# Performance work log

Measured on AMD Instinct MI355X. Metric: run time of the kernel, lower is better.

## Reference

```python
import jax, jax.numpy as jnp
import numpy as np

N = 20000
E = 320000
NEG_SLOPE = 0.2
BN_EPS = 1e-5


def _segment_softmax(e, dst, n):
    # e: [E, H] attention logits, dst: [E] destination node ids
    m = jax.ops.segment_max(e, dst, num_segments=n)           # [N, H]
    ex = jnp.exp(e - m[dst])                                   # [E, H]
    s = jax.ops.segment_sum(ex, dst, num_segments=n)          # [N, H]
    return ex / s[dst]


def gat_conv(x, src, dst, W, a_src, a_dst, b, heads, out_ch):
    # PyG GATConv (concat=True): h = x @ W reshaped to [N, H, C]
    n = x.shape[0]
    h = (x @ W).reshape(n, heads, out_ch)                      # [N, H, C]
    al_s = jnp.einsum('nhc,hc->nh', h, a_src)                  # [N, H]
    al_d = jnp.einsum('nhc,hc->nh', h, a_dst)
    e = jax.nn.leaky_relu(al_s[src] + al_d[dst], NEG_SLOPE)    # [E, H]
    alpha = _segment_softmax(e, dst, n)                        # [E, H]
    msg = h[src] * alpha[:, :, None]                           # [E, H, C]
    out = jax.ops.segment_sum(msg, dst, num_segments=n)        # [N, H, C]
    return out.reshape(n, heads * out_ch) + b


def batch_norm(x, gamma, beta):
    mu = jnp.mean(x, axis=0)
    var = jnp.mean((x - mu) ** 2, axis=0)  # biased, as torch BN training
    return gamma * (x - mu) * jax.lax.rsqrt(var + BN_EPS) + beta


def setup_inputs() -> dict:
    key = jax.random.key(0)
    ks = jax.random.split(key, 16)
    F_in, H1, C1 = 128, 8, 64
    D = H1 * C1  # 512
    OUT = 2
    def gl(k, shape, fan):
        return jax.random.normal(k, shape, dtype=jnp.float32) / np.sqrt(fan)
    x = jax.random.normal(ks[0], (N, F_in), dtype=jnp.float32)
    edge_index = jax.random.randint(ks[1], (2, E), 0, N, dtype=jnp.int64)
    return {
        'x': x, 'edge_index': edge_index,
        'W1': gl(ks[2], (F_in, H1 * C1), F_in),
        'a1s': gl(ks[3], (H1, C1), C1), 'a1d': gl(ks[4], (H1, C1), C1),
        'b1': jnp.zeros((D,), jnp.float32),
        'W2': gl(ks[5], (D, D), D),
        'a2s': gl(ks[6], (1, D), D), 'a2d': gl(ks[7], (1, D), D),
        'b2': jnp.zeros((D,), jnp.float32),
        'fc1_w': gl(ks[8], (D, D), D), 'fc1_b': jnp.zeros((D,), jnp.float32),
        'g1': jnp.ones((D,), jnp.float32), 'be1': jnp.zeros((D,), jnp.float32),
        'fc2_w': gl(ks[9], (D, D), D), 'fc2_b': jnp.zeros((D,), jnp.float32),
        'g2': jnp.ones((D,), jnp.float32), 'be2': jnp.zeros((D,), jnp.float32),
        'lin_w': gl(ks[10], (D, OUT), D), 'lin_b': jnp.zeros((OUT,), jnp.float32),
    }


def reference(x, edge_index, W1, a1s, a1d, b1, W2, a2s, a2d, b2,
              fc1_w, fc1_b, g1, be1, fc2_w, fc2_b, g2, be2, lin_w, lin_b):
    n = x.shape[0]
    loop = jnp.arange(n, dtype=edge_index.dtype)
    src = jnp.concatenate([edge_index[0], loop])  # add self-loops (PyG default)
    dst = jnp.concatenate([edge_index[1], loop])
    h = gat_conv(x, src, dst, W1, a1s, a1d, b1, heads=8, out_ch=64)
    h = batch_norm(jax.nn.relu(h @ fc1_w + fc1_b), g1, be1)
    h = gat_conv(h, src, dst, W2, a2s, a2d, b2, heads=1, out_ch=512)
    h = batch_norm(jax.nn.relu(h @ fc2_w + fc2_b), g2, be2)
    out = jax.nn.relu(h @ lin_w + lin_b)  # dropout p=0 is identity
    return out
```

## Files before the change

kernel.cpp:

```cpp
#include <hip/hip_runtime.h>
#include <hip/hip_bf16.h>

static constexpr int NN = 20000;
static constexpr int EE = 320000;
static constexpr int ET = EE + NN;
static constexpr int DD = 512;
static constexpr int FIN = 128;

typedef __attribute__((ext_vector_type(8))) short short8;
typedef __attribute__((ext_vector_type(4))) float f32x4;

__device__ __forceinline__ unsigned short f2bf(float f) {
    unsigned u = __float_as_uint(f);
    u += 0x7fffu + ((u >> 16) & 1u);
    return (unsigned short)(u >> 16);
}
__device__ __forceinline__ float bf2f(unsigned short b) {
    return __uint_as_float(((unsigned)b) << 16);
}

__device__ __forceinline__ void async_copy16(short* lds, const unsigned short* g) {
    __builtin_amdgcn_global_load_lds(
        (const __attribute__((address_space(1))) unsigned int*)g,
        (__attribute__((address_space(3))) unsigned int*)lds,
        16, 0, 0);
}

template <int IS64>
__global__ void count_deg(const void* __restrict__ ei, int* __restrict__ deg) {
    int i = blockIdx.x * blockDim.x + threadIdx.x;
    if (i >= EE) return;
    int d = IS64 ? (int)((const long long*)ei)[EE + i] : ((const int*)ei)[EE + i];
    atomicAdd(&deg[d], 1);
}

__global__ void scan_k(const int* __restrict__ deg, int* __restrict__ row_ptr) {
    __shared__ int part[1024];
    int t = threadIdx.x;
    const int CH = (NN + 1023) / 1024;
    int start = t * CH;
    int end = min(start + CH, NN);
    int s = 0;
    for (int i = start; i < end; ++i) s += deg[i] + 1;
    part[t] = s;
    __syncthreads();
    for (int off = 1; off < 1024; off <<= 1) {
        int v = 0;
        if (t >= off) v = part[t - off];
        __syncthreads();
        part[t] += v;
        __syncthreads();
    }
    int base = (t == 0) ? 0 : part[t - 1];
    for (int i = start; i < end; ++i) { row_ptr[i] = base; base += deg[i] + 1; }
    if (t == 1023) row_ptr[NN] = part[1023];
}

template <int IS64>
__global__ void fill_csr(const void* __restrict__ ei,
                         const int* __restrict__ row_ptr, int* __restrict__ cursor,
                         int* __restrict__ csr_src) {
    int e = blockIdx.x * blockDim.x + threadIdx.x;
    if (e >= ET) return;
    int s, d;
    if (e < EE) {
        if (IS64) {
            const long long* p = (const long long*)ei;
            s = (int)p[e]; d = (int)p[EE + e];
        } else {
            const int* p = (const int*)ei;
            s = p[e]; d = p[EE + e];
        }
    } else {
        s = d = e - EE;
    }
    int pos = atomicAdd(&cursor[d], 1);
    csr_src[row_ptr[d] + pos] = s;
}

static constexpr int TBLK = 208;
static constexpr int SZ_X = NN * FIN;
__global__ __launch_bounds__(256) void prep_all_k(
    const float* __restrict__ x, const float* __restrict__ W1,
    const float* __restrict__ fc1, const float* __restrict__ W2,
    const float* __restrict__ fc2,
    unsigned short* __restrict__ xb, unsigned short* __restrict__ W1t,
    unsigned short* __restrict__ fc1t, unsigned short* __restrict__ W2t,
    unsigned short* __restrict__ fc2t) {
    int b = blockIdx.x;
    if (b < TBLK) {
        __shared__ unsigned short tile[64][65];
        const float* src; unsigned short* dst; int rows, cols;
        if (b < 16)       { src = W1;  dst = W1t;  rows = FIN; cols = DD; }
        else if (b < 80)  { b -= 16;  src = fc1; dst = fc1t; rows = DD; cols = DD; }
        else if (b < 144) { b -= 80;  src = W2;  dst = W2t;  rows = DD; cols = DD; }
        else              { b -= 144; src = fc2; dst = fc2t; rows = DD; cols = DD; }
        int tc = cols / 64;
        int r0 = (b / tc) * 64, c0 = (b % tc) * 64;
        int t = threadIdx.x, lr = t >> 6, lc = t & 63;
#pragma unroll
        for (int p = 0; p < 16; ++p) {
            int r = lr + p * 4;
            tile[r][lc] = f2bf(src[(size_t)(r0 + r) * cols + c0 + lc]);
        }
        __syncthreads();
#pragma unroll
        for (int p = 0; p < 16; ++p) {
            int r = lr + p * 4;
            dst[(size_t)(c0 + r) * rows + r0 + lc] = tile[lc][r];
        }
        return;
    }
    int i = (b - TBLK) * 256 + threadIdx.x;
    if (i < SZ_X) xb[i] = f2bf(x[i]);
}

template <int RELU, int HASBIAS, int STATS, int ALS, int H>
__global__ __launch_bounds__(256) void gemm_bf16(const unsigned short* __restrict__ A,
                                                 const unsigned short* __restrict__ Bt,
                                                 const float* __restrict__ bias,
                                                 unsigned short* __restrict__ Cb,
                                                 float* __restrict__ bnstat,
                                                 const float* __restrict__ avs,
                                                 const float* __restrict__ avd,
                                                 float* __restrict__ al_s,
                                                 float* __restrict__ al_d,
                                                 int M, int Nc, int K) {
    int id = blockIdx.x;
    int bm = ((id >> 5) << 3) + (id & 7);
    int bn = (id >> 3) & 3;
    int m0 = bm * 128, n0 = bn * 128;
    if (m0 >= M) return;

    __shared__ short As0[128 * 32], As1[128 * 32];
    __shared__ short Bs0[128 * 32], Bs1[128 * 32];
    int t = threadIdx.x;
    int lane = t & 63, w = t >> 6;
    int wm = w & 1, wn = w >> 1;
    int quad = lane >> 4, mr = lane & 15;
    int lrow = lane >> 2;
    int lcol = (lane & 3) * 8;

    const unsigned short* Ag0 = A + (size_t)(m0 + w * 32 + lrow) * K + lcol;
    const unsigned short* Ag1 = A + (size_t)(m0 + w * 32 + 16 + lrow) * K + lcol;
    const unsigned short* Bg0 = Bt + (size_t)(n0 + w * 32 + lrow) * K + lcol;
    const unsigned short* Bg1 = Bt + (size_t)(n0 + w * 32 + 16 + lrow) * K + lcol;
    short* Al[2][2] = {{&As0[(w * 32) * 32], &As0[(w * 32 + 16) * 32]},
                       {&As1[(w * 32) * 32], &As1[(w * 32 + 16) * 32]}};
    short* Bl[2][2] = {{&Bs0[(w * 32) * 32], &Bs0[(w * 32 + 16) * 32]},
                       {&Bs1[(w * 32) * 32], &Bs1[(w * 32 + 16) * 32]}};

    f32x4 zero = {0.f, 0.f, 0.f, 0.f};
    f32x4 acc[4][4];
#pragma unroll
    for (int i = 0; i < 4; ++i)
#pragma unroll
        for (int j = 0; j < 4; ++j) acc[i][j] = zero;

    for (int k0 = 0; k0 < K; k0 += 64) {
        async_copy16(Al[0][0], Ag0 + k0);
        async_copy16(Al[1][0], Ag0 + k0 + 32);
        async_copy16(Al[0][1], Ag1 + k0);
        async_copy16(Al[1][1], Ag1 + k0 + 32);
        async_copy16(Bl[0][0], Bg0 + k0);
        async_copy16(Bl[1][0], Bg0 + k0 + 32);
        async_copy16(Bl[0][1], Bg1 + k0);
        async_copy16(Bl[1][1], Bg1 + k0 + 32);
        __syncthreads();
#pragma unroll
        for (int kp = 0; kp < 2; ++kp) {
            const short* Sa = kp ? As1 : As0;
            const short* Sb = kp ? Bs1 : Bs0;
            short8 af[4], bfr[4];
#pragma unroll
            for (int i = 0; i < 4; ++i) {
                af[i]  = *(const short8*)(&Sa[(wm * 64 + i * 16 + mr) * 32 + quad * 8]);
                bfr[i] = *(const short8*)(&Sb[(wn * 64 + i * 16 + mr) * 32 + quad * 8]);
            }
#pragma unroll
            for (int i = 0; i < 4; ++i)
#pragma unroll
                for (int j = 0; j < 4; ++j)
                    acc[i][j] = __builtin_amdgcn_mfma_f32_16x16x32_bf16(af[i], bfr[j], acc[i][j], 0, 0, 0);
        }
        __syncthreads();
    }

    float as_j[4], ad_j[4];
    if (ALS) {
#pragma unroll
        for (int j = 0; j < 4; ++j) {
            int n = n0 + wn * 64 + j * 16 + mr;
            as_j[j] = avs[n];
            ad_j[j] = avd[n];
        }
    }
    const int head = (H == 8) ? ((n0 + wn * 64) >> 6) : 0;
    float sj[4] = {0.f, 0.f, 0.f, 0.f}, qj[4] = {0.f, 0.f, 0.f, 0.f};
#pragma unroll
    for (int i = 0; i < 4; ++i) {
        int mb = m0 + wm * 64 + i * 16 + quad * 4;
#pragma unroll
        for (int r = 0; r < 4; ++r) {
            int m = mb + r;
            bool valid = (m < M);
            float ps = 0.f, pd = 0.f;
#pragma unroll
            for (int j = 0; j < 4; ++j) {
                int n = n0 + wn * 64 + j * 16 + mr;
                float v = acc[i][j][r];
                if (HASBIAS) v += bias[n];
                if (RELU) v = fmaxf(v, 0.f);
                unsigned short hb = f2bf(v);
                if (valid) Cb[(size_t)m * Nc + n] = hb;
                if (ALS) {
                    float vv = bf2f(hb);
                    ps += as_j[j] * vv;
                    pd += ad_j[j] * vv;
                }
                if (STATS && valid) { sj[j] += v; qj[j] += v * v; }
            }
            if (ALS) {
                ps += __shfl_xor(ps, 1); pd += __shfl_xor(pd, 1);
                ps += __shfl_xor(ps, 2); pd += __shfl_xor(pd, 2);
                ps += __shfl_xor(ps, 4); pd += __shfl_xor(pd, 4);
                ps += __shfl_xor(ps, 8); pd += __shfl_xor(pd, 8);
                if (mr == 0 && valid) {
                    if (H == 8) { al_s[m * 8 + head] = ps; al_d[m * 8 + head] = pd; }
                    else        { atomicAdd(&al_s[m], ps); atomicAdd(&al_d[m], pd); }
                }
            }
        }
    }
    if (STATS) {
#pragma unroll
        for (int j = 0; j < 4; ++j) {
            float s = sj[j], q = qj[j];
            s += __shfl_xor(s, 16); q += __shfl_xor(q, 16);
            s += __shfl_xor(s, 32); q += __shfl_xor(q, 32);
            if (lane < 16) {
                int n = n0 + wn * 64 + j * 16 + mr;
                atomicAdd(&bnstat[n], s);
                atomicAdd(&bnstat[512 + n], q);
            }
        }
    }
}

template <int H>
__global__ __launch_bounds__(256) void gat_gather_k(const unsigned short* __restrict__ hb,
                                                    const float* __restrict__ al_s,
                                                    const float* __restrict__ al_d,
                                                    const int* __restrict__ row_ptr,
                                                    const int* __restrict__ csr_src,
                                                    const float* __restrict__ bias,
                                                    unsigned short* __restrict__ outb) {
    int b = blockIdx.x;
    int slice = (b & 7) >> 1;
    int g = ((b >> 3) << 1) | (b & 1);
    int t = threadIdx.x;
    int w = t >> 6, lane = t & 63;
    int n = g * 4 + w;
    int col = slice * 128 + lane * 2;
    const int hh = (H == 8) ? (col >> 6) : 0;
    float ald = al_d[n * H + hh];
    int beg = row_ptr[n], end = row_ptr[n + 1];
    const char* hbase = (const char*)(hb + col);
    float acc0 = 0.f, acc1 = 0.f, psum = 0.f;

    for (int p0 = beg; p0 < end; p0 += 64) {
        int cnt = min(64, end - p0);
        int sv = (p0 + lane < end) ? csr_src[p0 + lane] : 0;
        int p = 0;
        for (; p + 8 <= cnt; p += 8) {
            int sn[8];
#pragma unroll
            for (int u = 0; u < 8; ++u) sn[u] = __shfl(sv, p + u);
            float l[8];
#pragma unroll
            for (int u = 0; u < 8; ++u) l[u] = al_s[sn[u] * H + hh] + ald;
            unsigned hv[8];
#pragma unroll
            for (int u = 0; u < 8; ++u)
                hv[u] = *(const unsigned*)(hbase + ((unsigned)sn[u] << 10));
            float a[8];
#pragma unroll
            for (int u = 0; u < 8; ++u) {
                float xx = l[u];
                a[u] = __expf((xx > 0.f) ? xx : 0.2f * xx);
                psum += a[u];
            }
#pragma unroll
            for (int u = 0; u < 8; ++u) {
                acc0 = fmaf(a[u], __uint_as_float(hv[u] << 16), acc0);
                acc1 = fmaf(a[u], __uint_as_float(hv[u] & 0xffff0000u), acc1);
            }
        }
        for (; p < cnt; ++p) {
            int sn0 = __shfl(sv, p);
            float l0 = al_s[sn0 * H + hh] + ald;
            unsigned h0 = *(const unsigned*)(hbase + ((unsigned)sn0 << 10));
            float a0 = __expf((l0 > 0.f) ? l0 : 0.2f * l0);
            psum += a0;
            acc0 = fmaf(a0, __uint_as_float(h0 << 16), acc0);
            acc1 = fmaf(a0, __uint_as_float(h0 & 0xffff0000u), acc1);
        }
    }
    float inv = 1.0f / psum;
    float2 bv = *(const float2*)(bias + col);
    unsigned short o0 = f2bf(acc0 * inv + bv.x);
    unsigned short o1 = f2bf(acc1 * inv + bv.y);
    *(unsigned*)(outb + (size_t)n * DD + col) = ((unsigned)o1 << 16) | (unsigned)o0;
}

__global__ __launch_bounds__(256) void fold1_k(const float* __restrict__ stat,
                                               const float* __restrict__ g,
                                               const float* __restrict__ be,
                                               unsigned short* __restrict__ W2t,
                                               float* __restrict__ bias2) {
    int t = threadIdx.x;
    int n = blockIdx.x * 4 + (t >> 6);
    int lane = t & 63;
    float pb = 0.f;
#pragma unroll
    for (int j = 0; j < 8; ++j) {
        int k = lane * 8 + j;
        float mean = stat[k] * (1.0f / NN);
        float var = stat[512 + k] * (1.0f / NN) - mean * mean;
        float sc = g[k] * rsqrtf(var + 1e-5f);
        float sh = be[k] - mean * sc;
        float wv = bf2f(W2t[n * DD + k]);
        W2t[n * DD + k] = f2bf(sc * wv);
        pb += sh * wv;
    }
    for (int off = 32; off; off >>= 1) pb += __shfl_down(pb, off);
    if (lane == 0) bias2[n] = pb;
}

__global__ void final_linear(const unsigned short* __restrict__ xb,
                             const float* __restrict__ stat, const float* __restrict__ g,
                             const float* __restrict__ be, const float* __restrict__ w,
                             const float* __restrict__ b, float* __restrict__ out) {
    int wave = (blockIdx.x * blockDim.x + threadIdx.x) >> 6;
    int lane = threadIdx.x & 63;
    if (wave >= NN) return;
    short8 hv = *(const short8*)(xb + (size_t)wave * DD + lane * 8);
    float p0 = 0.f, p1 = 0.f;
#pragma unroll
    for (int j = 0; j < 8; ++j) {
        int c = lane * 8 + j;
        float mean = stat[c] * (1.0f / NN);
        float var = stat[512 + c] * (1.0f / NN) - mean * mean;
        float sc = g[c] * rsqrtf(var + 1e-5f);
        float vn = (bf2f((unsigned short)hv[j]) - mean) * sc + be[c];
        p0 += vn * w[2 * c];
        p1 += vn * w[2 * c + 1];
    }
    for (int off = 32; off; off >>= 1) {
        p0 += __shfl_down(p0, off);
        p1 += __shfl_down(p1, off);
    }
    if (lane == 0) {
        out[wave * 2 + 0] = fmaxf(p0 + b[0], 0.f);
        out[wave * 2 + 1] = fmaxf(p1 + b[1], 0.f);
    }
}

extern "C" void kernel_launch(void* const* d_in, const int* in_sizes, int n_in,
                              void* d_out, int out_size, void* d_ws, size_t ws_size,
                              hipStream_t stream) {
    const float* x     = (const float*)d_in[0];
    const void*  ei    = d_in[1];
    const float* W1    = (const float*)d_in[2];
    const float* a1s   = (const float*)d_in[3];
    const float* a1d   = (const float*)d_in[4];
    const float* b1    = (const float*)d_in[5];
    const float* W2    = (const float*)d_in[6];
    const float* a2s   = (const float*)d_in[7];
    const float* a2d   = (const float*)d_in[8];
    const float* b2    = (const float*)d_in[9];
    const float* fc1_w = (const float*)d_in[10];
    const float* fc1_b = (const float*)d_in[11];
    const float* g1    = (const float*)d_in[12];
    const float* be1   = (const float*)d_in[13];
    const float* fc2_w = (const float*)d_in[14];
    const float* fc2_b = (const float*)d_in[15];
    const float* g2    = (const float*)d_in[16];
    const float* be2   = (const float*)d_in[17];
    const float* lin_w = (const float*)d_in[18];
    const float* lin_b = (const float*)d_in[19];
    float* out = (float*)d_out;

    char* ws = (char*)d_ws;
    auto alloc = [&](size_t bytes) {
        void* p = (void*)ws;
        ws += (bytes + 255) & ~size_t(255);
        return p;
    };
    unsigned short* h_bf    = (unsigned short*)alloc((size_t)NN * DD * 2);
    unsigned short* act_bf  = (unsigned short*)alloc((size_t)NN * DD * 2);
    unsigned short* W1t     = (unsigned short*)alloc((size_t)DD * FIN * 2);
    unsigned short* fc1t    = (unsigned short*)alloc((size_t)DD * DD * 2);
    unsigned short* W2t     = (unsigned short*)alloc((size_t)DD * DD * 2);
    unsigned short* fc2t    = (unsigned short*)alloc((size_t)DD * DD * 2);
    float*          al_s    = (float*)alloc((size_t)NN * 8 * 4);
    float*          al_d    = (float*)alloc((size_t)NN * 8 * 4);
    float*          al_s2   = (float*)alloc((size_t)NN * 4);
    float*          al_d2   = (float*)alloc((size_t)NN * 4);
    int*            row_ptr = (int*)alloc((size_t)(NN + 1) * 4);
    int*            deg     = (int*)alloc((size_t)NN * 4);
    int*            cursor  = (int*)alloc((size_t)NN * 4);
    int*            csr_src = (int*)alloc((size_t)ET * 4);
    float*          bnstatA = (float*)alloc(1024 * 4);
    float*          bnstatB = (float*)alloc(1024 * 4);
    float*          bias2f  = (float*)alloc(512 * 4);

    const int is64 = (in_sizes[1] >= (int)(2u * EE * 8u)) ? 1 : 0;

    hipMemsetAsync(deg, 0, (size_t)NN * 4, stream);
    hipMemsetAsync(cursor, 0, (size_t)NN * 4, stream);
    hipMemsetAsync(bnstatA, 0, 1024 * 4, stream);
    hipMemsetAsync(bnstatB, 0, 1024 * 4, stream);
    hipMemsetAsync(al_s2, 0, (size_t)NN * 4, stream);
    hipMemsetAsync(al_d2, 0, (size_t)NN * 4, stream);

    if (is64) {
        count_deg<1><<<(EE + 255) / 256, 256, 0, stream>>>(ei, deg);
    } else {
        count_deg<0><<<(EE + 255) / 256, 256, 0, stream>>>(ei, deg);
    }
    scan_k<<<1, 1024, 0, stream>>>(deg, row_ptr);
    if (is64) {
        fill_csr<1><<<(ET + 255) / 256, 256, 0, stream>>>(ei, row_ptr, cursor, csr_src);
    } else {
        fill_csr<0><<<(ET + 255) / 256, 256, 0, stream>>>(ei, row_ptr, cursor, csr_src);
    }

    unsigned short* x_bf = act_bf;
    const int prep_blocks = TBLK + (SZ_X + 255) / 256;
    prep_all_k<<<prep_blocks, 256, 0, stream>>>(x, W1, fc1_w, W2, fc2_w,
                                                x_bf, W1t, fc1t, W2t, fc2t);

    const int GB = 640;
    const int GGB = NN / 4 * 4;

    gemm_bf16<0, 0, 0, 1, 8><<<GB, 256, 0, stream>>>(
        x_bf, W1t, nullptr, h_bf, nullptr, a1s, a1d, al_s, al_d, NN, DD, FIN);
    gat_gather_k<8><<<GGB, 256, 0, stream>>>(h_bf, al_s, al_d, row_ptr, csr_src, b1, act_bf);
    gemm_bf16<1, 1, 1, 0, 8><<<GB, 256, 0, stream>>>(
        act_bf, fc1t, fc1_b, h_bf, bnstatA, nullptr, nullptr, nullptr, nullptr, NN, DD, DD);
    fold1_k<<<128, 256, 0, stream>>>(bnstatA, g1, be1, W2t, bias2f);

    gemm_bf16<0, 1, 0, 1, 1><<<GB, 256, 0, stream>>>(
        h_bf, W2t, bias2f, act_bf, nullptr, a2s, a2d, al_s2, al_d2, NN, DD, DD);
    gat_gather_k<1><<<GGB, 256, 0, stream>>>(act_bf, al_s2, al_d2, row_ptr, csr_src, b2, h_bf);
    gemm_bf16<1, 1, 1, 0, 8><<<GB, 256, 0, stream>>>(
        h_bf, fc2t, fc2_b, act_bf, bnstatB, nullptr, nullptr, nullptr, nullptr, NN, DD, DD);

    final_linear<<<(NN + 3) / 4, 256, 0, stream>>>(act_bf, bnstatB, g2, be2, lin_w, lin_b, out);
}
```

Measured before the change: 383.8 us.

## Precompute per-edge attention weights and parallelize gather across edges with wide loads

Adds kernels that compute the exponentiated leaky-relu attention weight for each CSR edge once, storing (src, weight) pairs per head, instead of recomputing them per column slice inside the gather. The gather kernel is restructured so each wave splits edges into 8 strips and columns into 8-element groups, using 16-byte feature loads and a cross-lane shuffle reduction. This removes redundant logit and exp work and improves memory-level parallelism. In exchange it adds an extra pass, a csr_dst array and a large edge-weight buffer that must be written and reread.

```diff
diff --git a/kernel.cpp b/kernel.cpp
--- a/kernel.cpp
+++ b/kernel.cpp
@@ -59,7 +59,7 @@
 template <int IS64>
 __global__ void fill_csr(const void* __restrict__ ei,
                          const int* __restrict__ row_ptr, int* __restrict__ cursor,
-                         int* __restrict__ csr_src) {
+                         int* __restrict__ csr_src, int* __restrict__ csr_dst) {
     int e = blockIdx.x * blockDim.x + threadIdx.x;
     if (e >= ET) return;
     int s, d;
@@ -75,7 +75,9 @@
         s = d = e - EE;
     }
     int pos = atomicAdd(&cursor[d], 1);
-    csr_src[row_ptr[d] + pos] = s;
+    int slot = row_ptr[d] + pos;
+    csr_src[slot] = s;
+    csr_dst[slot] = d;
 }
 
 static constexpr int TBLK = 208;
@@ -247,70 +249,82 @@
     }
 }
 
+__global__ __launch_bounds__(256) void alpha1_k(const float* __restrict__ al_s,
+                                                const float* __restrict__ al_d,
+                                                const int* __restrict__ csr_src,
+                                                const int* __restrict__ csr_dst,
+                                                int2* __restrict__ ea) {
+    int p = blockIdx.x * blockDim.x + threadIdx.x;
+    if (p >= ET) return;
+    int sn = csr_src[p], d = csr_dst[p];
+    float4 s0 = *(const float4*)(al_s + (size_t)sn * 8);
+    float4 s1 = *(const float4*)(al_s + (size_t)sn * 8 + 4);
+    float4 d0 = *(const float4*)(al_d + (size_t)d * 8);
+    float4 d1 = *(const float4*)(al_d + (size_t)d * 8 + 4);
+    float l[8] = {s0.x + d0.x, s0.y + d0.y, s0.z + d0.z, s0.w + d0.w,
+                  s1.x + d1.x, s1.y + d1.y, s1.z + d1.z, s1.w + d1.w};
+#pragma unroll
+    for (int h = 0; h < 8; ++h) {
+        float xx = l[h];
+        float a = __expf((xx > 0.f) ? xx : 0.2f * xx);
+        ea[(size_t)h * ET + p] = make_int2(sn, __float_as_int(a));
+    }
+}
+
+__global__ __launch_bounds__(256) void alpha2_k(const float* __restrict__ al_s,
+                                                const float* __restrict__ al_d,
+                                                const int* __restrict__ csr_src,
+                                                const int* __restrict__ csr_dst,
+                                                int2* __restrict__ ea) {
+    int p = blockIdx.x * blockDim.x + threadIdx.x;
+    if (p >= ET) return;
+    int sn = csr_src[p], d = csr_dst[p];
+    float xx = al_s[sn] + al_d[d];
+    float a = __expf((xx > 0.f) ? xx : 0.2f * xx);
+    ea[p] = make_int2(sn, __float_as_int(a));
+}
+
 template <int H>
 __global__ __launch_bounds__(256) void gat_gather_k(const unsigned short* __restrict__ hb,
-                                                    const float* __restrict__ al_s,
-                                                    const float* __restrict__ al_d,
+                                                    const int2* __restrict__ ea,
                                                     const int* __restrict__ row_ptr,
-                                                    const int* __restrict__ csr_src,
                                                     const float* __restrict__ bias,
                                                     unsigned short* __restrict__ outb) {
     int b = blockIdx.x;
-    int slice = (b & 7) >> 1;
-    int g = ((b >> 3) << 1) | (b & 1);
+    int s = b & 7;
+    int g = b >> 3;
     int t = threadIdx.x;
     int w = t >> 6, lane = t & 63;
     int n = g * 4 + w;
-    int col = slice * 128 + lane * 2;
-    const int hh = (H == 8) ? (col >> 6) : 0;
-    float ald = al_d[n * H + hh];
+    int estrip = lane >> 3, cg = lane & 7;
+    int col = s * 64 + cg * 8;
+    const int2* ep = ea + (H == 8 ? (size_t)s * ET : 0);
     int beg = row_ptr[n], end = row_ptr[n + 1];
-    const char* hbase = (const char*)(hb + col);
-    float acc0 = 0.f, acc1 = 0.f, psum = 0.f;
-
-    for (int p0 = beg; p0 < end; p0 += 64) {
-        int cnt = min(64, end - p0);
-        int sv = (p0 + lane < end) ? csr_src[p0 + lane] : 0;
-        int p = 0;
-        for (; p + 8 <= cnt; p += 8) {
-            int sn[8];
-#pragma unroll
-            for (int u = 0; u < 8; ++u) sn[u] = __shfl(sv, p + u);
-            float l[8];
-#pragma unroll
-            for (int u = 0; u < 8; ++u) l[u] = al_s[sn[u] * H + hh] + ald;
-            unsigned hv[8];
-#pragma unroll
-            for (int u = 0; u < 8; ++u)
-                hv[u] = *(const unsigned*)(hbase + ((unsigned)sn[u] << 10));
-            float a[8];
-#pragma unroll
-            for (int u = 0; u < 8; ++u) {
-                float xx = l[u];
-                a[u] = __expf((xx > 0.f) ? xx : 0.2f * xx);
-                psum += a[u];
-            }
-#pragma unroll
-            for (int u = 0; u < 8; ++u) {
-                acc0 = fmaf(a[u], __uint_as_float(hv[u] << 16), acc0);
-                acc1 = fmaf(a[u], __uint_as_float(hv[u] & 0xffff0000u), acc1);
-            }
-        }
-        for (; p < cnt; ++p) {
-            int sn0 = __shfl(sv, p);
-            float l0 = al_s[sn0 * H + hh] + ald;
-            unsigned h0 = *(const unsigned*)(hbase + ((unsigned)sn0 << 10));
-            float a0 = __expf((l0 > 0.f) ? l0 : 0.2f * l0);
-            psum += a0;
-            acc0 = fmaf(a0, __uint_as_float(h0 << 16), acc0);
-            acc1 = fmaf(a0, __uint_as_float(h0 & 0xffff0000u), acc1);
-        }
-    }
-    float inv = 1.0f / psum;
-    float2 bv = *(const float2*)(bias + col);
-    unsigned short o0 = f2bf(acc0 * inv + bv.x);
-    unsigned short o1 = f2bf(acc1 * inv + bv.y);
-    *(unsigned*)(outb + (size_t)n * DD + col) = ((unsigned)o1 << 16) | (unsigned)o0;
+
+    float acc[8] = {0.f, 0.f, 0.f, 0.f, 0.f, 0.f, 0.f, 0.f};
+    float psum = 0.f;
+    for (int p = beg + estrip; p < end; p += 8) {
+        int2 v = ep[p];
+        float a = __int_as_float(v.y);
+        psum += a;
+        short8 hv = *(const short8*)(hb + ((size_t)v.x << 9) + col);
+#pragma unroll
+        for (int j = 0; j < 8; ++j)
+            acc[j] = fmaf(a, bf2f((unsigned short)hv[j]), acc[j]);
+    }
+#pragma unroll
+    for (int m = 8; m <= 32; m <<= 1) {
+        psum += __shfl_xor(psum, m);
+#pragma unroll
+        for (int j = 0; j < 8; ++j) acc[j] += __shfl_xor(acc[j], m);
+    }
+    if (estrip == 0) {
+        float inv = 1.0f / psum;
+        unsigned short ov[8];
+#pragma unroll
+        for (int j = 0; j < 8; ++j) ov[j] = f2bf(acc[j] * inv + bias[col + j]);
+        *(int4*)(outb + (size_t)n * DD + col) = *(const int4*)ov;
+    }
 }
 
 __global__ __launch_bounds__(256) void fold1_k(const float* __restrict__ stat,
@@ -411,9 +425,11 @@
     int*            deg     = (int*)alloc((size_t)NN * 4);
     int*            cursor  = (int*)alloc((size_t)NN * 4);
     int*            csr_src = (int*)alloc((size_t)ET * 4);
+    int*            csr_dst = (int*)alloc((size_t)ET * 4);
     float*          bnstatA = (float*)alloc(1024 * 4);
     float*          bnstatB = (float*)alloc(1024 * 4);
     float*          bias2f  = (float*)alloc(512 * 4);
+    int2*           ea      = (int2*)alloc((size_t)8 * ET * 8);
 
     const int is64 = (in_sizes[1] >= (int)(2u * EE * 8u)) ? 1 : 0;
 
@@ -431,9 +447,9 @@
     }
     scan_k<<<1, 1024, 0, stream>>>(deg, row_ptr);
     if (is64) {
-        fill_csr<1><<<(ET + 255) / 256, 256, 0, stream>>>(ei, row_ptr, cursor, csr_src);
+        fill_csr<1><<<(ET + 255) / 256, 256, 0, stream>>>(ei, row_ptr, cursor, csr_src, csr_dst);
     } else {
-        fill_csr<0><<<(ET + 255) / 256, 256, 0, stream>>>(ei, row_ptr, cursor, csr_src);
+        fill_csr<0><<<(ET + 255) / 256, 256, 0, stream>>>(ei, row_ptr, cursor, csr_src, csr_dst);
     }
 
     unsigned short* x_bf = act_bf;
@@ -442,18 +458,21 @@
                                                 x_bf, W1t, fc1t, W2t, fc2t);
 
     const int GB = 640;
-    const int GGB = NN / 4 * 4;
+    const int GGB = 8 * (NN / 4);
+    const int AB = (ET + 255) / 256;
 
     gemm_bf16<0, 0, 0, 1, 8><<<GB, 256, 0, stream>>>(
         x_bf, W1t, nullptr, h_bf, nullptr, a1s, a1d, al_s, al_d, NN, DD, FIN);
-    gat_gather_k<8><<<GGB, 256, 0, stream>>>(h_bf, al_s, al_d, row_ptr, csr_src, b1, act_bf);
+    alpha1_k<<<AB, 256, 0, stream>>>(al_s, al_d, csr_src, csr_dst, ea);
+    gat_gather_k<8><<<GGB, 256, 0, stream>>>(h_bf, ea, row_ptr, b1, act_bf);
     gemm_bf16<1, 1, 1, 0, 8><<<GB, 256, 0, stream>>>(
         act_bf, fc1t, fc1_b, h_bf, bnstatA, nullptr, nullptr, nullptr, nullptr, NN, DD, DD);
     fold1_k<<<128, 256, 0, stream>>>(bnstatA, g1, be1, W2t, bias2f);
 
     gemm_bf16<0, 1, 0, 1, 1><<<GB, 256, 0, stream>>>(
         h_bf, W2t, bias2f, act_bf, nullptr, a2s, a2d, al_s2, al_d2, NN, DD, DD);
-    gat_gather_k<1><<<GGB, 256, 0, stream>>>(act_bf, al_s2, al_d2, row_ptr, csr_src, b2, h_bf);
+    alpha2_k<<<AB, 256, 0, stream>>>(al_s2, al_d2, csr_src, csr_dst, ea);
+    gat_gather_k<1><<<GGB, 256, 0, stream>>>(act_bf, ea, row_ptr, b2, h_bf);
     gemm_bf16<1, 1, 1, 0, 8><<<GB, 256, 0, stream>>>(
         h_bf, fc2t, fc2_b, act_bf, bnstatB, nullptr, nullptr, nullptr, nullptr, NN, DD, DD);
 
```

New measurement: 415.9 us. +8.4%, slower.
